# Optimization experiments

Hardware: AMD Instinct MI355X
Metric: run time of the kernel (lower is better)

## Reference

```python
import jax, jax.numpy as jnp
import numpy as np

B = 64          # batch
LS = 1024       # Nt * N
LW = 1024       # beamformer length
LY = 2048       # measurement length
M = 16          # number of sensors
N_STEP = 10     # unrolled update steps
MODULUS = 1.0
D = 2 * LS + 2 * LW + LY   # 6144, MLP input dim
H = 512                    # MLP hidden dim


def setup_inputs() -> dict:
    key = jax.random.key(0)
    ks = jax.random.split(key, 18)
    r = lambda k, shp, s: jax.random.normal(k, shp, dtype=jnp.float32) * s
    W_SCALE = 0.02  # keep the unrolled recursion numerically stable
    return {
        "phi0_batch": jax.random.uniform(ks[0], (B, LS), dtype=jnp.float32,
                                         minval=-np.pi, maxval=np.pi),
        "w_M_re": r(ks[1], (B, LW, M), 1.0),
        "w_M_im": r(ks[2], (B, LW, M), 1.0),
        "y_M": r(ks[3], (LY, M), 1.0),
        # est_eta_modules: D -> H -> LS
        "eW1": r(ks[4], (D, H), W_SCALE), "eb1": jnp.zeros((H,), jnp.float32),
        "eW2": r(ks[5], (H, LS), W_SCALE), "eb2": jnp.zeros((LS,), jnp.float32),
        # est_rho_modules: D -> H -> 1
        "rW1": r(ks[6], (D, H), W_SCALE), "rb1": jnp.zeros((H,), jnp.float32),
        "rW2": r(ks[7], (H, 1), W_SCALE), "rb2": jnp.zeros((1,), jnp.float32),
        # est_mu_modules: D -> H -> 1
        "mW1": r(ks[8], (D, H), W_SCALE), "mb1": jnp.zeros((H,), jnp.float32),
        "mW2": r(ks[9], (H, 1), W_SCALE), "mb2": jnp.zeros((1,), jnp.float32),
    }


def _mlp(x, W1, b1, W2, b2):
    return jax.nn.relu(x @ W1 + b1) @ W2 + b2


def _forward(phi0, w_re, w_im, y,
             eW1, eb1, eW2, eb2, rW1, rb1, rW2, rb2, mW1, mb1, mW2, mb2):
    # per-(batch, sensor) static features
    wr = jnp.swapaxes(w_re, 1, 2)                       # [B, M, LW]
    wi = jnp.swapaxes(w_im, 1, 2)                       # [B, M, LW]
    yt = jnp.broadcast_to(y.T[None], (phi0.shape[0], M, LY))  # [B, M, LY]

    def step(phi, _):
        s = MODULUS * jnp.exp(1j * phi)                 # [B, LS] complex64
        sr = jnp.broadcast_to(s.real[:, None, :], (phi.shape[0], M, LS))
        si = jnp.broadcast_to(s.imag[:, None, :], (phi.shape[0], M, LS))
        x = jnp.concatenate([sr, si, wr, wi, yt], axis=-1)  # [B, M, D]
        eta = _mlp(x, eW1, eb1, eW2, eb2)               # [B, M, LS]
        rho = _mlp(x, rW1, rb1, rW2, rb2)               # [B, M, 1]
        mu = _mlp(x, mW1, mb1, mW2, mb2)                # [B, M, 1]
        eta_net = jnp.sum(mu * rho * eta, axis=1)       # [B, LS]
        return phi - eta_net, s

    phi_f, s_seq = jax.lax.scan(step, phi0, None, length=N_STEP)
    s_last = MODULUS * jnp.exp(1j * phi_f)              # [B, LS]
    # [B, N_STEP+1, LS]
    return jnp.concatenate([jnp.moveaxis(s_seq, 0, 1), s_last[:, None, :]], axis=1)


def reference(phi0_batch, w_M_re, w_M_im, y_M,
              eW1, eb1, eW2, eb2, rW1, rb1, rW2, rb2, mW1, mb1, mW2, mb2):
    s_stack = _forward(phi0_batch, w_M_re, w_M_im, y_M,
                       eW1, eb1, eW2, eb2, rW1, rb1, rW2, rb2,
                       mW1, mb1, mW2, mb2)
    # complex output represented as stacked (real, imag): [B, N_STEP+1, LS, 2]
    s_ri = jnp.stack([s_stack.real, s_stack.imag], axis=-1)
    # faithful to original: mu_stack_batch is allocated but never written
    mu_stack = jnp.zeros((phi0_batch.shape[0], N_STEP, M), jnp.float32)
    return (s_ri, mu_stack)
```

## Files before the change

### kernel.cpp

```cpp
#include <hip/hip_runtime.h>
#include <math.h>

#define OFF_PHI    0u
#define SZ_PHI     (64u*1024u)
#define OFF_CS     (OFF_PHI + SZ_PHI)
#define SZ_CS      (64u*2048u)
#define OFF_STAT   (OFF_CS + SZ_CS)
#define SZ_STAT    (3u*1024u*512u)
#define OFF_SCR    (OFF_STAT + SZ_STAT)
#define OFF_STATP1 OFF_SCR
#define OFF_YPART  (OFF_STATP1 + SZ_STAT)
#define OFF_YSTAT  (OFF_YPART + 3u*8u*16u*512u)
#define OFF_DYNP   OFF_SCR
#define OFF_HW     (OFF_DYNP + 48u*64u*512u)
#define OFF_SUMC   (OFF_HW + 64u*512u)
#define OFF_ETAP   (OFF_SUMC + 64u)

#define OUT_S_FLOATS (64u*11u*1024u*2u)

__global__ __launch_bounds__(512) void k_ystat_part(
    const float* __restrict__ y,
    const float* __restrict__ eW1, const float* __restrict__ rW1,
    const float* __restrict__ mW1, float* __restrict__ ypart) {
  int mlp = blockIdx.x, m = blockIdx.y, slab = blockIdx.z, h = threadIdx.x;
  const float* W1 = (mlp == 0) ? eW1 : (mlp == 1) ? rW1 : mW1;
  int k0 = slab * 256;
  const float* Wp = W1 + (size_t)(4096 + k0) * 512 + h;
  const float* yp = y + (size_t)k0 * 16 + m;
  float acc = 0.f;
  #pragma unroll 8
  for (int l = 0; l < 256; ++l)
    acc = fmaf(yp[l * 16], Wp[(size_t)l * 512], acc);
  ypart[(((size_t)mlp * 8 + slab) * 16 + m) * 512 + h] = acc;
}

__global__ __launch_bounds__(512) void k_ystat_red(
    const float* __restrict__ ypart,
    const float* __restrict__ eb1, const float* __restrict__ rb1,
    const float* __restrict__ mb1, float* __restrict__ ystat) {
  int mlp = blockIdx.x, m = blockIdx.y, h = threadIdx.x;
  const float* b1 = (mlp == 0) ? eb1 : (mlp == 1) ? rb1 : mb1;
  float acc = b1[h];
  #pragma unroll
  for (int s = 0; s < 8; ++s)
    acc += ypart[(((size_t)mlp * 8 + s) * 16 + m) * 512 + h];
  ystat[((size_t)mlp * 16 + m) * 512 + h] = acc;
}

__global__ __launch_bounds__(256) void k_static_gemm(
    const float* __restrict__ wre, const float* __restrict__ wim,
    const float* __restrict__ eW1, const float* __restrict__ rW1,
    const float* __restrict__ mW1,
    float* __restrict__ statp0, float* __restrict__ statp1) {
  int mlp = blockIdx.z >> 1, khalf = blockIdx.z & 1;
  const float* W1 = (mlp == 0) ? eW1 : (mlp == 1) ? rW1 : mW1;
  const float* src = khalf ? wim : wre;
  int m0 = blockIdx.x * 64, n0 = blockIdx.y * 64;
  int b0 = m0 >> 4;
  const float* Bbase = W1 + (size_t)(2048 + 1024 * khalf) * 512 + n0;

  __shared__ float As[2][32][68];
  __shared__ float Bs[2][32][64];
  int tid = threadIdx.x;
  int ty = tid >> 4, tx = tid & 15;

  int a_ab0 = tid >> 7, a_al = (tid >> 2) & 31, a_am4 = (tid & 3) << 2;
  int b_br = tid >> 4, b_bn4 = (tid & 15) << 2;

  const float* ApG0 = src + ((size_t)(b0 + a_ab0)     * 1024 + a_al) * 16 + a_am4;
  const float* ApG1 = src + ((size_t)(b0 + a_ab0 + 2) * 1024 + a_al) * 16 + a_am4;
  const float* BpG0 = Bbase + (size_t)b_br * 512 + b_bn4;
  const float* BpG1 = Bbase + (size_t)(b_br + 16) * 512 + b_bn4;
  float4 a0 = *(const float4*)(ApG0);
  float4 a1 = *(const float4*)(ApG1);
  float4 bv0 = *(const float4*)(BpG0);
  float4 bv1 = *(const float4*)(BpG1);

  float acc[4][4] = {};
  int buf = 0;
  for (int kk = 0; kk < 1024; kk += 32) {
    *(float4*)&As[buf][a_al][(a_ab0 << 4) + a_am4] = a0;
    *(float4*)&As[buf][a_al][((a_ab0 + 2) << 4) + a_am4] = a1;
    *(float4*)&Bs[buf][b_br][b_bn4] = bv0;
    *(float4*)&Bs[buf][b_br + 16][b_bn4] = bv1;
    __syncthreads();
    int kn = (kk + 32 < 1024) ? kk + 32 : kk;
    a0 = *(const float4*)(ApG0 + (size_t)kn * 16);
    a1 = *(const float4*)(ApG1 + (size_t)kn * 16);
    bv0 = *(const float4*)(BpG0 + (size_t)kn * 512);
    bv1 = *(const float4*)(BpG1 + (size_t)kn * 512);
    #pragma unroll
    for (int k = 0; k < 32; ++k) {
      float4 a = *(const float4*)&As[buf][k][ty << 2];
      float4 bb = *(const float4*)&Bs[buf][k][tx << 2];
      float ar[4] = {a.x, a.y, a.z, a.w};
      float br[4] = {bb.x, bb.y, bb.z, bb.w};
      #pragma unroll
      for (int i = 0; i < 4; ++i)
        #pragma unroll
        for (int j = 0; j < 4; ++j)
          acc[i][j] = fmaf(ar[i], br[j], acc[i][j]);
    }
    buf ^= 1;
  }
  float* statp = khalf ? statp1 : statp0;
  #pragma unroll
  for (int i = 0; i < 4; ++i) {
    int bm = m0 + (ty << 2) + i;
    float* cp = statp + ((size_t)mlp * 1024 + bm) * 512 + n0 + (tx << 2);
    #pragma unroll
    for (int j = 0; j < 4; ++j) cp[j] = acc[i][j];
  }
}

__global__ __launch_bounds__(256) void k_stat_red(
    float* __restrict__ statp0, const float* __restrict__ statp1,
    const float* __restrict__ ystat) {
  unsigned f4 = blockIdx.x * 256 + threadIdx.x;
  size_t flat = (size_t)f4 * 4;
  unsigned mlp = flat >> 19;
  unsigned rem = flat & ((1u << 19) - 1);
  unsigned bm = rem >> 9, h = rem & 511;
  float4 v0 = *(const float4*)(statp0 + flat);
  float4 v1 = *(const float4*)(statp1 + flat);
  float4 ys = *(const float4*)(ystat + ((size_t)mlp * 16 + (bm & 15)) * 512 + h);
  v0.x += v1.x + ys.x; v0.y += v1.y + ys.y;
  v0.z += v1.z + ys.z; v0.w += v1.w + ys.w;
  *(float4*)(statp0 + flat) = v0;
}

__global__ __launch_bounds__(256) void k_dyn(
    const float* __restrict__ A,
    const float* __restrict__ B0, const float* __restrict__ B1,
    const float* __restrict__ B2, float* __restrict__ C) {
  const float* Bm = (blockIdx.z == 0) ? B0 : (blockIdx.z == 1) ? B1 : B2;
  int n0 = blockIdx.x * 64;
  int kbase = blockIdx.y * 128;
  __shared__ float As[2][16][68];
  __shared__ float Bs[2][16][64];
  int tid = threadIdx.x;
  int ty = tid >> 4, tx = tid & 15;
  int arow = tid >> 2, akk = (tid & 3) << 2;
  int bkk = tid >> 4, bnn = (tid & 15) << 2;
  const float* Ap = A + (size_t)arow * 2048 + kbase + akk;
  const float* Bp = Bm + ((size_t)(kbase + bkk)) * 512 + n0 + bnn;
  float4 av = *(const float4*)(Ap);
  float4 bv = *(const float4*)(Bp);
  float acc[4][4] = {};
  int buf = 0;
  for (int k0 = 0; k0 < 128; k0 += 16) {
    As[buf][akk + 0][arow] = av.x; As[buf][akk + 1][arow] = av.y;
    As[buf][akk + 2][arow] = av.z; As[buf][akk + 3][arow] = av.w;
    *(float4*)&Bs[buf][bkk][bnn] = bv;
    __syncthreads();
    int kn = (k0 + 16 < 128) ? k0 + 16 : k0;
    av = *(const float4*)(Ap + kn);
    bv = *(const float4*)(Bp + (size_t)kn * 512);
    #pragma unroll
    for (int k = 0; k < 16; ++k) {
      float4 a = *(const float4*)&As[buf][k][ty << 2];
      float4 bb = *(const float4*)&Bs[buf][k][tx << 2];
      float ar[4] = {a.x, a.y, a.z, a.w};
      float br[4] = {bb.x, bb.y, bb.z, bb.w};
      #pragma unroll
      for (int i = 0; i < 4; ++i)
        #pragma unroll
        for (int j = 0; j < 4; ++j)
          acc[i][j] = fmaf(ar[i], br[j], acc[i][j]);
    }
    buf ^= 1;
  }
  int chunk = blockIdx.y * 3 + blockIdx.z;
  float* Cp = C + ((size_t)chunk * 64) * 512 + n0;
  #pragma unroll
  for (int i = 0; i < 4; ++i)
    #pragma unroll
    for (int j = 0; j < 4; ++j)
      Cp[((size_t)((ty << 2) + i)) * 512 + (tx << 2) + j] = acc[i][j];
}

__global__ __launch_bounds__(512) void k_reduce(
    const float* __restrict__ dynp, const float* __restrict__ stat,
    const float* __restrict__ rW2, const float* __restrict__ rb2,
    const float* __restrict__ mW2, const float* __restrict__ mb2,
    float* __restrict__ hw, float* __restrict__ sumc) {
  int b = blockIdx.x, h = threadIdx.x;
  float de = 0.f, dr = 0.f, dm = 0.f;
  #pragma unroll
  for (int s = 0; s < 16; ++s) {
    de += dynp[((size_t)((s * 3 + 0) * 64 + b)) * 512 + h];
    dr += dynp[((size_t)((s * 3 + 1) * 64 + b)) * 512 + h];
    dm += dynp[((size_t)((s * 3 + 2) * 64 + b)) * 512 + h];
  }
  float wr2 = rW2[h], wm2 = mW2[h];
  int lane = h & 63, wave = h >> 6;
  __shared__ float s_r[16][8], s_m[16][8], s_c[16];
  const float* se_p = stat + ((size_t)(0 * 1024) + b * 16) * 512 + h;
  const float* sr_p = stat + ((size_t)(1 * 1024) + b * 16) * 512 + h;
  const float* sm_p = stat + ((size_t)(2 * 1024) + b * 16) * 512 + h;
  float he[16];
  #pragma unroll
  for (int m = 0; m < 16; ++m) {
    he[m] = fmaxf(de + se_p[(size_t)m * 512], 0.f);
    float hr = fmaxf(dr + sr_p[(size_t)m * 512], 0.f);
    float hm = fmaxf(dm + sm_p[(size_t)m * 512], 0.f);
    float pr = hr * wr2, pm = hm * wm2;
    #pragma unroll
    for (int off = 32; off; off >>= 1) {
      pr += __shfl_down(pr, off);
      pm += __shfl_down(pm, off);
    }
    if (lane == 0) { s_r[m][wave] = pr; s_m[m][wave] = pm; }
  }
  __syncthreads();
  if (h < 16) {
    int m = h;
    float rho = rb2[0], mu = mb2[0];
    #pragma unroll
    for (int w = 0; w < 8; ++w) { rho += s_r[m][w]; mu += s_m[m][w]; }
    float coeff = rho * mu;
    s_c[m] = coeff;
    float t = coeff;
    #pragma unroll
    for (int off = 8; off; off >>= 1) t += __shfl_down(t, off);
    if (m == 0) sumc[b] = t;
  }
  __syncthreads();
  float hwacc = 0.f;
  #pragma unroll
  for (int m = 0; m < 16; ++m) hwacc = fmaf(s_c[m], he[m], hwacc);
  hw[(size_t)b * 512 + h] = hwacc;
}

__global__ __launch_bounds__(256) void k_etap(
    const float* __restrict__ hw, const float* __restrict__ eW2,
    float* __restrict__ etap) {
  int n0 = blockIdx.x * 64;
  int kbase = blockIdx.y * 64;
  __shared__ float As[2][16][68];
  __shared__ float Bs[2][16][64];
  int tid = threadIdx.x;
  int ty = tid >> 4, tx = tid & 15;
  int arow = tid >> 2, akk = (tid & 3) << 2;
  int bkk = tid >> 4, bnn = (tid & 15) << 2;
  const float* Ap = hw + (size_t)arow * 512 + kbase + akk;
  const float* Bp = eW2 + (size_t)(kbase + bkk) * 1024 + n0 + bnn;
  float4 av = *(const float4*)(Ap);
  float4 bv = *(const float4*)(Bp);
  float acc[4][4] = {};
  int buf = 0;
  for (int k0 = 0; k0 < 64; k0 += 16) {
    As[buf][akk + 0][arow] = av.x; As[buf][akk + 1][arow] = av.y;
    As[buf][akk + 2][arow] = av.z; As[buf][akk + 3][arow] = av.w;
    *(float4*)&Bs[buf][bkk][bnn] = bv;
    __syncthreads();
    int kn = (k0 + 16 < 64) ? k0 + 16 : k0;
    av = *(const float4*)(Ap + kn);
    bv = *(const float4*)(Bp + (size_t)kn * 1024);
    #pragma unroll
    for (int k = 0; k < 16; ++k) {
      float4 a = *(const float4*)&As[buf][k][ty << 2];
      float4 bb = *(const float4*)&Bs[buf][k][tx << 2];
      float ar[4] = {a.x, a.y, a.z, a.w};
      float br[4] = {bb.x, bb.y, bb.z, bb.w};
      #pragma unroll
      for (int i = 0; i < 4; ++i)
        #pragma unroll
        for (int j = 0; j < 4; ++j)
          acc[i][j] = fmaf(ar[i], br[j], acc[i][j]);
    }
    buf ^= 1;
  }
  float* Cp = etap + ((size_t)blockIdx.y * 64) * 1024 + n0;
  #pragma unroll
  for (int i = 0; i < 4; ++i)
    #pragma unroll
    for (int j = 0; j < 4; ++j)
      Cp[((size_t)((ty << 2) + i)) * 1024 + (tx << 2) + j] = acc[i][j];
}

__global__ __launch_bounds__(256) void k_update(
    const float* __restrict__ etap, const float* __restrict__ eb2,
    const float* __restrict__ sumc, float* __restrict__ phi,
    float* __restrict__ cs, float* __restrict__ out, int t) {
  int i = blockIdx.x * 256 + threadIdx.x;
  int b = i >> 10, k = i & 1023;
  float e = sumc[b] * eb2[k];
  #pragma unroll
  for (int s = 0; s < 8; ++s)
    e += etap[((size_t)(s * 64 + b)) * 1024 + k];
  float p = phi[i] - e;
  phi[i] = p;
  float sn, cn;
  sincosf(p, &sn, &cn);
  cs[(size_t)b * 2048 + k] = cn;
  cs[(size_t)b * 2048 + 1024 + k] = sn;
  size_t o = (((size_t)(b * 11 + t + 1)) * 1024 + k) * 2;
  out[o] = cn; out[o + 1] = sn;
}

__global__ __launch_bounds__(256) void k_init(
    const float* __restrict__ phi0, float* __restrict__ phi,
    float* __restrict__ cs, float* __restrict__ out) {
  int bid = blockIdx.x;
  if (bid < 256) {
    int i = bid * 256 + threadIdx.x;
    float p = phi0[i];
    phi[i] = p;
    int b = i >> 10, k = i & 1023;
    float sn, cn;
    sincosf(p, &sn, &cn);
    cs[(size_t)b * 2048 + k] = cn;
    cs[(size_t)b * 2048 + 1024 + k] = sn;
    size_t o = (((size_t)b * 11) * 1024 + k) * 2;
    out[o] = cn; out[o + 1] = sn;
  } else {
    int j = (bid - 256) * 256 + threadIdx.x;
    out[OUT_S_FLOATS + j] = 0.f;
  }
}

extern "C" void kernel_launch(void* const* d_in, const int* in_sizes, int n_in,
                              void* d_out, int out_size, void* d_ws, size_t ws_size,
                              hipStream_t stream) {
  const float* phi0 = (const float*)d_in[0];
  const float* wre  = (const float*)d_in[1];
  const float* wim  = (const float*)d_in[2];
  const float* y    = (const float*)d_in[3];
  const float* eW1  = (const float*)d_in[4];
  const float* eb1  = (const float*)d_in[5];
  const float* eW2  = (const float*)d_in[6];
  const float* eb2  = (const float*)d_in[7];
  const float* rW1  = (const float*)d_in[8];
  const float* rb1  = (const float*)d_in[9];
  const float* rW2  = (const float*)d_in[10];
  const float* rb2  = (const float*)d_in[11];
  const float* mW1  = (const float*)d_in[12];
  const float* mb1  = (const float*)d_in[13];
  const float* mW2  = (const float*)d_in[14];
  const float* mb2  = (const float*)d_in[15];

  float* ws     = (float*)d_ws;
  float* phi    = ws + OFF_PHI;
  float* cs     = ws + OFF_CS;
  float* stat   = ws + OFF_STAT;
  float* statp1 = ws + OFF_STATP1;
  float* ypart  = ws + OFF_YPART;
  float* ystat  = ws + OFF_YSTAT;
  float* dynp   = ws + OFF_DYNP;
  float* hw     = ws + OFF_HW;
  float* sumc   = ws + OFF_SUMC;
  float* etap   = ws + OFF_ETAP;
  float* out    = (float*)d_out;

  k_ystat_part<<<dim3(3, 16, 8), dim3(512), 0, stream>>>(y, eW1, rW1, mW1, ypart);
  k_ystat_red<<<dim3(3, 16), dim3(512), 0, stream>>>(ypart, eb1, rb1, mb1, ystat);
  k_static_gemm<<<dim3(16, 8, 6), dim3(256), 0, stream>>>(
      wre, wim, eW1, rW1, mW1, stat, statp1);
  k_stat_red<<<dim3(1536), dim3(256), 0, stream>>>(stat, statp1, ystat);
  k_init<<<dim3(296), dim3(256), 0, stream>>>(phi0, phi, cs, out);

  for (int t = 0; t < 10; ++t) {
    k_dyn<<<dim3(8, 16, 3), dim3(256), 0, stream>>>(cs, eW1, rW1, mW1, dynp);
    k_reduce<<<dim3(64), dim3(512), 0, stream>>>(
        dynp, stat, rW2, rb2, mW2, mb2, hw, sumc);
    k_etap<<<dim3(16, 8), dim3(256), 0, stream>>>(hw, eW2, etap);
    k_update<<<dim3(256), dim3(256), 0, stream>>>(
        etap, eb2, sumc, phi, cs, out, t);
  }
}
```

Measured before the change: 543.7 us.

## Fuse eta GEMM with phase update into one per-batch GEMV kernel

Replaces the split-K tiled GEMM that wrote eight partial eta slabs, and the separate update kernel that summed them, with one kernel. Each block stages one batch row of hw in shared memory and computes a GEMV over eW2 for 256 outputs, then applies the phi update and sincos directly. This removes one launch per step and the partial-sum round trip through global memory. In exchange eW2 (2 MB) is re-read by all 64 batch rows, relying on L2 rather than register tiling for reuse, and each thread runs a 512-long serial reduction.

```diff
diff --git a/kernel.cpp b/kernel.cpp
--- a/kernel.cpp
+++ b/kernel.cpp
@@ -14,7 +14,6 @@
 #define OFF_DYNP   OFF_SCR
 #define OFF_HW     (OFF_DYNP + 48u*64u*512u)
 #define OFF_SUMC   (OFF_HW + 64u*512u)
-#define OFF_ETAP   (OFF_SUMC + 64u)
 
 #define OUT_S_FLOATS (64u*11u*1024u*2u)
 
@@ -232,70 +231,34 @@
   hw[(size_t)b * 512 + h] = hwacc;
 }
 
-__global__ __launch_bounds__(256) void k_etap(
+__global__ __launch_bounds__(256) void k_eta_update(
     const float* __restrict__ hw, const float* __restrict__ eW2,
-    float* __restrict__ etap) {
-  int n0 = blockIdx.x * 64;
-  int kbase = blockIdx.y * 64;
-  __shared__ float As[2][16][68];
-  __shared__ float Bs[2][16][64];
-  int tid = threadIdx.x;
-  int ty = tid >> 4, tx = tid & 15;
-  int arow = tid >> 2, akk = (tid & 3) << 2;
-  int bkk = tid >> 4, bnn = (tid & 15) << 2;
-  const float* Ap = hw + (size_t)arow * 512 + kbase + akk;
-  const float* Bp = eW2 + (size_t)(kbase + bkk) * 1024 + n0 + bnn;
-  float4 av = *(const float4*)(Ap);
-  float4 bv = *(const float4*)(Bp);
-  float acc[4][4] = {};
-  int buf = 0;
-  for (int k0 = 0; k0 < 64; k0 += 16) {
-    As[buf][akk + 0][arow] = av.x; As[buf][akk + 1][arow] = av.y;
-    As[buf][akk + 2][arow] = av.z; As[buf][akk + 3][arow] = av.w;
-    *(float4*)&Bs[buf][bkk][bnn] = bv;
-    __syncthreads();
-    int kn = (k0 + 16 < 64) ? k0 + 16 : k0;
-    av = *(const float4*)(Ap + kn);
-    bv = *(const float4*)(Bp + (size_t)kn * 1024);
-    #pragma unroll
-    for (int k = 0; k < 16; ++k) {
-      float4 a = *(const float4*)&As[buf][k][ty << 2];
-      float4 bb = *(const float4*)&Bs[buf][k][tx << 2];
-      float ar[4] = {a.x, a.y, a.z, a.w};
-      float br[4] = {bb.x, bb.y, bb.z, bb.w};
-      #pragma unroll
-      for (int i = 0; i < 4; ++i)
-        #pragma unroll
-        for (int j = 0; j < 4; ++j)
-          acc[i][j] = fmaf(ar[i], br[j], acc[i][j]);
-    }
-    buf ^= 1;
-  }
-  float* Cp = etap + ((size_t)blockIdx.y * 64) * 1024 + n0;
-  #pragma unroll
-  for (int i = 0; i < 4; ++i)
-    #pragma unroll
-    for (int j = 0; j < 4; ++j)
-      Cp[((size_t)((ty << 2) + i)) * 1024 + (tx << 2) + j] = acc[i][j];
-}
-
-__global__ __launch_bounds__(256) void k_update(
-    const float* __restrict__ etap, const float* __restrict__ eb2,
-    const float* __restrict__ sumc, float* __restrict__ phi,
-    float* __restrict__ cs, float* __restrict__ out, int t) {
-  int i = blockIdx.x * 256 + threadIdx.x;
-  int b = i >> 10, k = i & 1023;
-  float e = sumc[b] * eb2[k];
-  #pragma unroll
-  for (int s = 0; s < 8; ++s)
-    e += etap[((size_t)(s * 64 + b)) * 1024 + k];
-  float p = phi[i] - e;
-  phi[i] = p;
+    const float* __restrict__ eb2, const float* __restrict__ sumc,
+    float* __restrict__ phi, float* __restrict__ cs,
+    float* __restrict__ out, int t) {
+  int b = blockIdx.y;
+  int kg = blockIdx.x * 256 + threadIdx.x;
+  __shared__ float hws[512];
+  hws[threadIdx.x] = hw[(size_t)b * 512 + threadIdx.x];
+  hws[threadIdx.x + 256] = hw[(size_t)b * 512 + 256 + threadIdx.x];
+  __syncthreads();
+  const float* W = eW2 + kg;
+  float a0 = 0.f, a1 = 0.f, a2 = 0.f, a3 = 0.f;
+  #pragma unroll 4
+  for (int h = 0; h < 512; h += 4) {
+    a0 = fmaf(hws[h + 0], W[(size_t)(h + 0) * 1024], a0);
+    a1 = fmaf(hws[h + 1], W[(size_t)(h + 1) * 1024], a1);
+    a2 = fmaf(hws[h + 2], W[(size_t)(h + 2) * 1024], a2);
+    a3 = fmaf(hws[h + 3], W[(size_t)(h + 3) * 1024], a3);
+  }
+  float e = ((a0 + a1) + (a2 + a3)) + sumc[b] * eb2[kg];
+  float p = phi[(size_t)b * 1024 + kg] - e;
+  phi[(size_t)b * 1024 + kg] = p;
   float sn, cn;
   sincosf(p, &sn, &cn);
-  cs[(size_t)b * 2048 + k] = cn;
-  cs[(size_t)b * 2048 + 1024 + k] = sn;
-  size_t o = (((size_t)(b * 11 + t + 1)) * 1024 + k) * 2;
+  cs[(size_t)b * 2048 + kg] = cn;
+  cs[(size_t)b * 2048 + 1024 + kg] = sn;
+  size_t o = (((size_t)(b * 11 + t + 1)) * 1024 + kg) * 2;
   out[o] = cn; out[o + 1] = sn;
 }
 
@@ -350,7 +313,6 @@
   float* dynp   = ws + OFF_DYNP;
   float* hw     = ws + OFF_HW;
   float* sumc   = ws + OFF_SUMC;
-  float* etap   = ws + OFF_ETAP;
   float* out    = (float*)d_out;
 
   k_ystat_part<<<dim3(3, 16, 8), dim3(512), 0, stream>>>(y, eW1, rW1, mW1, ypart);
@@ -364,8 +326,7 @@
     k_dyn<<<dim3(8, 16, 3), dim3(256), 0, stream>>>(cs, eW1, rW1, mW1, dynp);
     k_reduce<<<dim3(64), dim3(512), 0, stream>>>(
         dynp, stat, rW2, rb2, mW2, mb2, hw, sumc);
-    k_etap<<<dim3(16, 8), dim3(256), 0, stream>>>(hw, eW2, etap);
-    k_update<<<dim3(256), dim3(256), 0, stream>>>(
-        etap, eb2, sumc, phi, cs, out, t);
-  }
-}
+    k_eta_update<<<dim3(4, 64), dim3(256), 0, stream>>>(
+        hw, eW2, eb2, sumc, phi, cs, out, t);
+  }
+}
```

Result: slower. 638.9 us (+17.5%).
